# Optimization experiments

Measured on AMD Instinct MI355X. Metric: run time of the kernel, lower is better.

## Reference

```python
import jax, jax.numpy as jnp
import numpy as np

# Static DAG: input -> L hidden layers of K nodes (dense between layers) -> output.
B, WIDTH, K, L = 262144, 64, 4, 4


def _linear_init(key, shape, fan_in):
    # matches nn.Linear default: U(-1/sqrt(fan_in), 1/sqrt(fan_in))
    bound = 1.0 / np.sqrt(fan_in)
    return jax.random.uniform(key, shape, jnp.float32, -bound, bound)


def setup_inputs() -> dict:
    key = jax.random.key(0)
    ks = jax.random.split(key, 9)
    x = jax.random.normal(ks[0], (B, WIDTH), jnp.float32)
    # input node -> first hidden layer (K edges)
    W_in = _linear_init(ks[1], (K, WIDTH, WIDTH), WIDTH)
    b_in = _linear_init(ks[2], (K, WIDTH), WIDTH)
    # between hidden layers: (L-1) transitions, K*K edges each; [pred, node, out, in]
    W_mid = _linear_init(ks[3], (L - 1, K, K, WIDTH, WIDTH), WIDTH)
    b_mid = _linear_init(ks[4], (L - 1, K, K, WIDTH), WIDTH)
    # last hidden layer -> output node (K edges)
    W_out = _linear_init(ks[5], (K, WIDTH, WIDTH), WIDTH)
    b_out = _linear_init(ks[6], (K, WIDTH), WIDTH)
    return {"x": x, "W_in": W_in, "b_in": b_in, "W_mid": W_mid,
            "b_mid": b_mid, "W_out": W_out, "b_out": b_out}


def _l2_normalize(t):
    # torch.linalg.norm(t) with no dim: Frobenius norm over the WHOLE tensor
    return t / jnp.linalg.norm(t)


def reference(x, W_in, b_in, W_mid, b_mid, W_out, b_out):
    # input node -> layer 1: each node k gets a single edge Linear, then normalize
    h = jnp.einsum('bw,kvw->kbv', x, W_in) + b_in[:, None, :]  # [K,B,W]
    h = jax.vmap(_l2_normalize)(h)
    # hidden -> hidden transitions: node v sums over its K predecessor edges
    for l in range(L - 1):  # small fixed structural loop over layers
        pre = jnp.einsum('pbw,pkvw->kbv', h, W_mid[l]) + b_mid[l].sum(axis=0)[:, None, :]
        h = jax.vmap(_l2_normalize)(pre)
    # last layer -> output node: sum K edge outputs, normalize
    out = jnp.einsum('pbw,pvw->bv', h, W_out) + b_out.sum(axis=0)
    return _l2_normalize(out)
```

## Files before the change

kernel.cpp:

```cpp
#include <hip/hip_runtime.h>


#define BF 262144.0f
#define SLOT 4608

#define OFF_G   0
#define OFF_S   4096
#define OFF_P2  8192
#define OFF_C2  73728
#define OFF_P4  74752
#define OFF_C4  91136
#define OFF_MO  91392
#define OFF_CO  95488
#define OFF_X16 98304

typedef __attribute__((ext_vector_type(8))) short bf16x8;
typedef __attribute__((ext_vector_type(4))) float f32x4;
typedef __attribute__((ext_vector_type(4))) unsigned short u16x4;

__device__ __forceinline__ unsigned short f2bf(float f) {
  unsigned u = __builtin_bit_cast(unsigned, f);
  u += 0x7FFF + ((u >> 16) & 1);
  return (unsigned short)(u >> 16);
}
__device__ __forceinline__ float bf2f(unsigned short h) {
  unsigned u = ((unsigned)h) << 16;
  return __builtin_bit_cast(float, u);
}

__device__ __forceinline__ bf16x8 cvt8(f32x4 a, f32x4 b, float s) {
  bf16x8 t;
#pragma unroll
  for (int j = 0; j < 4; j++) {
    t[j]     = (short)f2bf(a[j] * s);
    t[j + 4] = (short)f2bf(b[j] * s);
  }
  return t;
}

__device__ __forceinline__ void split8(f32x4 a, f32x4 b, float sc,
                                       bf16x8& hi, bf16x8& lo) {
#pragma unroll
  for (int j = 0; j < 4; j++) {
    float v = a[j] * sc;
    unsigned short h = f2bf(v);
    hi[j] = (short)h; lo[j] = (short)f2bf(v - bf2f(h));
    v = b[j] * sc;
    h = f2bf(v);
    hi[j + 4] = (short)h; lo[j + 4] = (short)f2bf(v - bf2f(h));
  }
}

__device__ __forceinline__ float qpart(const unsigned short* th,
                                       const unsigned short* tl,
                                       int it, int col, int quad,
                                       const float Greg[4][4]) {
  f32x4 dq[4];
#pragma unroll
  for (int ut = 0; ut < 4; ut++) dq[ut] = (f32x4){0.f, 0.f, 0.f, 0.f};
#pragma unroll
  for (int ks = 0; ks < 2; ks++) {
    const bf16x8 ah = *(const bf16x8*)&th[(it * 16 + col) * 72 + ks * 32 + quad * 8];
    const bf16x8 al = *(const bf16x8*)&tl[(it * 16 + col) * 72 + ks * 32 + quad * 8];
#pragma unroll
    for (int ut = 0; ut < 4; ut++) {
      const bf16x8 bh = *(const bf16x8*)&th[(ut * 16 + col) * 72 + ks * 32 + quad * 8];
      const bf16x8 bl = *(const bf16x8*)&tl[(ut * 16 + col) * 72 + ks * 32 + quad * 8];
      dq[ut] = __builtin_amdgcn_mfma_f32_16x16x32_bf16(ah, bh, dq[ut], 0, 0, 0);
      dq[ut] = __builtin_amdgcn_mfma_f32_16x16x32_bf16(ah, bl, dq[ut], 0, 0, 0);
      dq[ut] = __builtin_amdgcn_mfma_f32_16x16x32_bf16(al, bh, dq[ut], 0, 0, 0);
    }
  }
  float qp = 0.f;
#pragma unroll
  for (int ut = 0; ut < 4; ut++)
#pragma unroll
    for (int r = 0; r < 4; r++) qp += dq[ut][r] * Greg[ut][r];
  return qp;
}

__device__ __forceinline__ void blkred(float qp, float* red4, float* qvv,
                                       int idx, int tid, int lane, int it) {
#pragma unroll
  for (int off = 32; off; off >>= 1) qp += __shfl_down(qp, off, 64);
  if (lane == 0) red4[it] = qp;
  __syncthreads();
  if (tid == 0) qvv[idx] = 1.0f / sqrtf(red4[0] + red4[1] + red4[2] + red4[3]);
  __syncthreads();
}

__global__ __launch_bounds__(256) void kG(const float* __restrict__ x,
                                          float* __restrict__ Gpart,
                                          unsigned short* __restrict__ x16) {
  __shared__ __align__(16) unsigned short xts[4][4][16][8];
  __shared__ float sred[256][4];
  const int tid = threadIdx.x;
  const int lane = tid & 63, mt = tid >> 6;
  const int col = lane & 15, q = lane >> 4;
  const int row0 = tid >> 4;
  const int cf0  = (tid & 15) * 4;

  f32x4 acc[4];
#pragma unroll
  for (int nt = 0; nt < 4; nt++) acc[nt] = (f32x4){0.f, 0.f, 0.f, 0.f};
  float s0 = 0.f, s1 = 0.f, s2 = 0.f, s3 = 0.f;

  const long brow = (long)blockIdx.x * 512;
  const float* bx = x + brow * 64;
  f32x4 r0 = *(const f32x4*)(bx + tid * 4);
  f32x4 r1 = *(const f32x4*)(bx + 1024 + tid * 4);

  for (int c = 0; c < 16; c++) {
    __syncthreads();
    s0 += r0[0] + r1[0]; s1 += r0[1] + r1[1];
    s2 += r0[2] + r1[2]; s3 += r0[3] + r1[3];
    u16x4 h0, h1;
#pragma unroll
    for (int j = 0; j < 4; j++) {
      const int cf = cf0 + j;
      const unsigned short b0 = f2bf(r0[j]);
      const unsigned short b1 = f2bf(r1[j]);
      h0[j] = b0; h1[j] = b1;
      xts[cf >> 4][row0 >> 3][cf & 15][row0 & 7]        = b0;
      xts[cf >> 4][2 + (row0 >> 3)][cf & 15][row0 & 7]  = b1;
    }
    *(u16x4*)(x16 + (brow + c * 32 + row0) * 64 + cf0)      = h0;
    *(u16x4*)(x16 + (brow + c * 32 + 16 + row0) * 64 + cf0) = h1;
    f32x4 r0n = r0, r1n = r1;
    if (c < 15) {
      r0n = *(const f32x4*)(bx + (c + 1) * 2048 + tid * 4);
      r1n = *(const f32x4*)(bx + (c + 1) * 2048 + 1024 + tid * 4);
    }
    __syncthreads();
    const bf16x8 af = *(const bf16x8*)xts[mt][q][col];
#pragma unroll
    for (int nt = 0; nt < 4; nt++) {
      const bf16x8 bfr = *(const bf16x8*)xts[nt][q][col];
      acc[nt] = __builtin_amdgcn_mfma_f32_16x16x32_bf16(af, bfr, acc[nt], 0, 0, 0);
    }
    r0 = r0n; r1 = r1n;
  }

  float* myp = Gpart + (long)blockIdx.x * 4160;
#pragma unroll
  for (int nt = 0; nt < 4; nt++)
#pragma unroll
    for (int r = 0; r < 4; r++)
      myp[(mt * 16 + q * 4 + r) * 64 + nt * 16 + col] = acc[nt][r];

  sred[tid][0] = s0; sred[tid][1] = s1; sred[tid][2] = s2; sred[tid][3] = s3;
  __syncthreads();
  if (tid < 64) {
    float t = 0.f;
#pragma unroll
    for (int k2 = 0; k2 < 16; k2++) t += sred[(tid >> 2) + 16 * k2][tid & 3];
    myp[4096 + tid] = t;
  }
}

__global__ __launch_bounds__(256) void kGred(const float* __restrict__ Gpart,
                                             float* __restrict__ G,
                                             float* __restrict__ s) {
  __shared__ float red[4][64];
  const int tid = threadIdx.x;
  const int e = blockIdx.x * 64 + (tid & 63);
  const int quarter = tid >> 6;
  float acc = 0.f;
#pragma unroll 4
  for (int j = 0; j < 128; j++)
    acc += Gpart[(long)(quarter * 128 + j) * 4160 + e];
  red[quarter][tid & 63] = acc;
  __syncthreads();
  if (tid < 64) {
    const float t = red[0][tid] + red[1][tid] + red[2][tid] + red[3][tid];
    const int ee = blockIdx.x * 64 + tid;
    if (ee < 4096) G[ee] = t;
    else           s[ee - 4096] = t;
  }
}

__global__ __launch_bounds__(256) void kChainA(
    const float* __restrict__ Win, const float* __restrict__ bin,
    const float* __restrict__ Wm0, const float* __restrict__ bm0,
    const float* __restrict__ Wm1, const float* __restrict__ bm1,
    const float* __restrict__ G, const float* __restrict__ s,
    float* __restrict__ Pout, float* __restrict__ cpout) {
  extern __shared__ __align__(16) char smem[];
  unsigned short* Tth = (unsigned short*)smem;
  unsigned short* Ttl = Tth + 4 * SLOT;
  float* cAv  = (float*)(Ttl + 4 * SLOT);
  float* cBv  = cAv + 256;
  float* slv  = cBv + 64;
  float* red4 = slv + 64;
  float* qvv  = red4 + 4;
  float* Tf   = qvv + 8;

  const int tid = threadIdx.x;
  const int p2 = blockIdx.x >> 2, k2 = blockIdx.x & 3;
  const int lane = tid & 63, it = tid >> 6;
  const int col = lane & 15, quad = lane >> 4;

  float Greg[4][4];
#pragma unroll
  for (int ut = 0; ut < 4; ut++)
#pragma unroll
    for (int r = 0; r < 4; r++)
      Greg[ut][r] = G[(it * 16 + quad * 4 + r) * 64 + ut * 16 + col];
  if (tid < 64) slv[tid] = s[tid];
  if (tid < 256) cAv[tid] = bin[tid];

  for (int p = 0; p < 4; p++) {
#pragma unroll
    for (int m = 0; m < 4; m++) {
      const int li = m * 1024 + tid * 4;
      *(f32x4*)&Tf[(li >> 6) * 68 + (li & 63)] = *(const f32x4*)(Win + p * 4096 + li);
    }
    __syncthreads();
    const int tc = tid >> 2, rb = (tid & 3) * 16;
#pragma unroll
    for (int j = 0; j < 16; j++) {
      const float tv = Tf[(rb + j) * 68 + tc];
      const unsigned short h = f2bf(tv);
      Tth[p * SLOT + tc * 72 + rb + j] = h;
      Ttl[p * SLOT + tc * 72 + rb + j] = f2bf(tv - bf2f(h));
    }
    __syncthreads();
  }

#pragma unroll
  for (int p = 0; p < 4; p++) {
    float qp = qpart(Tth + p * SLOT, Ttl + p * SLOT, it, col, quad, Greg);
    if (tid < 64) {
      float sd = 0.f;
      for (int w = 0; w < 64; w++)
        sd += slv[w] * (bf2f(Tth[p * SLOT + w * 72 + tid]) +
                        bf2f(Ttl[p * SLOT + w * 72 + tid]));
      const float c = cAv[p * 64 + tid];
      qp += c * (2.f * sd + BF * c);
    }
    blkred(qp, red4, qvv, p, tid, lane, it);
  }

  f32x4 dc[4];
#pragma unroll
  for (int nt = 0; nt < 4; nt++) dc[nt] = (f32x4){0.f, 0.f, 0.f, 0.f};
  float c2acc = 0.f;

  const int arow = it * 16 + col;
  f32x4 wr[4];
  {
    const float* wbase = Wm0 + (long)((0 * 4 + p2) * 64 + arow) * 64;
    wr[0] = *(const f32x4*)(wbase + quad * 8);
    wr[1] = *(const f32x4*)(wbase + quad * 8 + 4);
    wr[2] = *(const f32x4*)(wbase + 32 + quad * 8);
    wr[3] = *(const f32x4*)(wbase + 36 + quad * 8);
  }
#pragma unroll
  for (int p = 0; p < 4; p++) {
    const float inv = qvv[p];
    bf16x8 awh0, awl0, awh1, awl1;
    split8(wr[0], wr[1], inv, awh0, awl0);
    split8(wr[2], wr[3], inv, awh1, awl1);
    if (p < 3) {
      const float* wbase = Wm0 + (long)(((p + 1) * 4 + p2) * 64 + arow) * 64;
      wr[0] = *(const f32x4*)(wbase + quad * 8);
      wr[1] = *(const f32x4*)(wbase + quad * 8 + 4);
      wr[2] = *(const f32x4*)(wbase + 32 + quad * 8);
      wr[3] = *(const f32x4*)(wbase + 36 + quad * 8);
    }
#pragma unroll
    for (int nt = 0; nt < 4; nt++) {
      const bf16x8 bh0 = *(const bf16x8*)&Tth[p * SLOT + (nt * 16 + col) * 72 + quad * 8];
      const bf16x8 bl0 = *(const bf16x8*)&Ttl[p * SLOT + (nt * 16 + col) * 72 + quad * 8];
      dc[nt] = __builtin_amdgcn_mfma_f32_16x16x32_bf16(awh0, bh0, dc[nt], 0, 0, 0);
      dc[nt] = __builtin_amdgcn_mfma_f32_16x16x32_bf16(awh0, bl0, dc[nt], 0, 0, 0);
      dc[nt] = __builtin_amdgcn_mfma_f32_16x16x32_bf16(awl0, bh0, dc[nt], 0, 0, 0);
      const bf16x8 bh1 = *(const bf16x8*)&Tth[p * SLOT + (nt * 16 + col) * 72 + 32 + quad * 8];
      const bf16x8 bl1 = *(const bf16x8*)&Ttl[p * SLOT + (nt * 16 + col) * 72 + 32 + quad * 8];
      dc[nt] = __builtin_amdgcn_mfma_f32_16x16x32_bf16(awh1, bh1, dc[nt], 0, 0, 0);
      dc[nt] = __builtin_amdgcn_mfma_f32_16x16x32_bf16(awh1, bl1, dc[nt], 0, 0, 0);
      dc[nt] = __builtin_amdgcn_mfma_f32_16x16x32_bf16(awl1, bh1, dc[nt], 0, 0, 0);
    }
    if (tid < 64) {
      const float* wrow = Wm0 + (long)((p * 4 + p2) * 64 + tid) * 64;
      float pc = 0.f;
#pragma unroll
      for (int u4 = 0; u4 < 16; u4++) {
        const f32x4 wv = *(const f32x4*)(wrow + u4 * 4);
        pc += wv[0] * cAv[p * 64 + u4 * 4]     + wv[1] * cAv[p * 64 + u4 * 4 + 1] +
              wv[2] * cAv[p * 64 + u4 * 4 + 2] + wv[3] * cAv[p * 64 + u4 * 4 + 3];
      }
      c2acc += inv * pc + bm0[(p * 4 + p2) * 64 + tid];
    }
  }
  __syncthreads();

#pragma unroll
  for (int nt = 0; nt < 4; nt++)
#pragma unroll
    for (int r = 0; r < 4; r++) {
      const float val = dc[nt][r];
      const unsigned short h = f2bf(val);
      const int w_ = nt * 16 + col, v_ = it * 16 + quad * 4 + r;
      Tth[w_ * 72 + v_] = h;
      Ttl[w_ * 72 + v_] = f2bf(val - bf2f(h));
    }
  if (tid < 64) cBv[tid] = c2acc;
  __syncthreads();

  {
    float qp = qpart(Tth, Ttl, it, col, quad, Greg);
    if (tid < 64) {
      float sd = 0.f;
      for (int w = 0; w < 64; w++)
        sd += slv[w] * (bf2f(Tth[w * 72 + tid]) + bf2f(Ttl[w * 72 + tid]));
      const float c = cBv[tid];
      qp += c * (2.f * sd + BF * c);
    }
    blkred(qp, red4, qvv, 4, tid, lane, it);
  }
  const float inv2 = qvv[4];

  {
    f32x4 dcO[4];
#pragma unroll
    for (int nt = 0; nt < 4; nt++) dcO[nt] = (f32x4){0.f, 0.f, 0.f, 0.f};
    const float* wbase = Wm1 + (long)((p2 * 4 + k2) * 64 + arow) * 64;
    const f32x4 w0 = *(const f32x4*)(wbase + quad * 8);
    const f32x4 w1 = *(const f32x4*)(wbase + quad * 8 + 4);
    const f32x4 w2 = *(const f32x4*)(wbase + 32 + quad * 8);
    const f32x4 w3 = *(const f32x4*)(wbase + 36 + quad * 8);
    bf16x8 awh0, awl0, awh1, awl1;
    split8(w0, w1, inv2, awh0, awl0);
    split8(w2, w3, inv2, awh1, awl1);
#pragma unroll
    for (int nt = 0; nt < 4; nt++) {
      const bf16x8 bh0 = *(const bf16x8*)&Tth[(nt * 16 + col) * 72 + quad * 8];
      const bf16x8 bl0 = *(const bf16x8*)&Ttl[(nt * 16 + col) * 72 + quad * 8];
      dcO[nt] = __builtin_amdgcn_mfma_f32_16x16x32_bf16(awh0, bh0, dcO[nt], 0, 0, 0);
      dcO[nt] = __builtin_amdgcn_mfma_f32_16x16x32_bf16(awh0, bl0, dcO[nt], 0, 0, 0);
      dcO[nt] = __builtin_amdgcn_mfma_f32_16x16x32_bf16(awl0, bh0, dcO[nt], 0, 0, 0);
      const bf16x8 bh1 = *(const bf16x8*)&Tth[(nt * 16 + col) * 72 + 32 + quad * 8];
      const bf16x8 bl1 = *(const bf16x8*)&Ttl[(nt * 16 + col) * 72 + 32 + quad * 8];
      dcO[nt] = __builtin_amdgcn_mfma_f32_16x16x32_bf16(awh1, bh1, dcO[nt], 0, 0, 0);
      dcO[nt] = __builtin_amdgcn_mfma_f32_16x16x32_bf16(awh1, bl1, dcO[nt], 0, 0, 0);
      dcO[nt] = __builtin_amdgcn_mfma_f32_16x16x32_bf16(awl1, bh1, dcO[nt], 0, 0, 0);
    }
    float* po = Pout + (long)(p2 * 4 + k2) * 4096;
#pragma unroll
    for (int nt = 0; nt < 4; nt++)
#pragma unroll
      for (int r = 0; r < 4; r++)
        po[(it * 16 + quad * 4 + r) * 64 + nt * 16 + col] = dcO[nt][r];
    if (tid < 64) {
      const float* wrow = Wm1 + (long)((p2 * 4 + k2) * 64 + tid) * 64;
      float pc = 0.f;
#pragma unroll
      for (int u4 = 0; u4 < 16; u4++) {
        const f32x4 wv = *(const f32x4*)(wrow + u4 * 4);
        pc += wv[0] * cBv[u4 * 4]     + wv[1] * cBv[u4 * 4 + 1] +
              wv[2] * cBv[u4 * 4 + 2] + wv[3] * cBv[u4 * 4 + 3];
      }
      cpout[(p2 * 4 + k2) * 64 + tid] = inv2 * pc + bm1[(p2 * 4 + k2) * 64 + tid];
    }
  }
}

__global__ __launch_bounds__(256) void kChainB(
    const float* __restrict__ Pin, const float* __restrict__ cpin,
    const float* __restrict__ Wm2, const float* __restrict__ bm2,
    const float* __restrict__ Wout, const float* __restrict__ bout,
    const float* __restrict__ G, const float* __restrict__ s,
    float* __restrict__ Pout, float* __restrict__ cpout) {
  extern __shared__ __align__(16) char smem[];
  unsigned short* Tth = (unsigned short*)smem;
  unsigned short* Ttl = Tth + 4 * SLOT;
  float* cAv  = (float*)(Ttl + 4 * SLOT);
  float* cBv  = cAv + 256;
  float* slv  = cBv + 64;
  float* red4 = slv + 64;
  float* qvv  = red4 + 4;
  float* Tf   = qvv + 8;

  const int tid = threadIdx.x;
  const int kp = blockIdx.x;
  const int lane = tid & 63, it = tid >> 6;
  const int col = lane & 15, quad = lane >> 4;

  float Greg[4][4];
#pragma unroll
  for (int ut = 0; ut < 4; ut++)
#pragma unroll
    for (int r = 0; r < 4; r++)
      Greg[ut][r] = G[(it * 16 + quad * 4 + r) * 64 + ut * 16 + col];
  if (tid < 64) slv[tid] = s[tid];
  if (tid < 256) {
    const int k = tid >> 6, v = tid & 63;
    cAv[tid] = cpin[(0 * 4 + k) * 64 + v] + cpin[(1 * 4 + k) * 64 + v] +
               cpin[(2 * 4 + k) * 64 + v] + cpin[(3 * 4 + k) * 64 + v];
  }

  for (int k = 0; k < 4; k++) {
#pragma unroll
    for (int m = 0; m < 4; m++) {
      const int li = m * 1024 + tid * 4;
      const f32x4 a = *(const f32x4*)(Pin + (0 * 4 + k) * 4096 + li);
      const f32x4 b = *(const f32x4*)(Pin + (1 * 4 + k) * 4096 + li);
      const f32x4 c = *(const f32x4*)(Pin + (2 * 4 + k) * 4096 + li);
      const f32x4 d = *(const f32x4*)(Pin + (3 * 4 + k) * 4096 + li);
      *(f32x4*)&Tf[(li >> 6) * 68 + (li & 63)] = a + b + c + d;
    }
    __syncthreads();
    const int tc = tid >> 2, rb = (tid & 3) * 16;
#pragma unroll
    for (int j = 0; j < 16; j++) {
      const float tv = Tf[(rb + j) * 68 + tc];
      const unsigned short h = f2bf(tv);
      Tth[k * SLOT + tc * 72 + rb + j] = h;
      Ttl[k * SLOT + tc * 72 + rb + j] = f2bf(tv - bf2f(h));
    }
    __syncthreads();
  }

#pragma unroll
  for (int k = 0; k < 4; k++) {
    float qp = qpart(Tth + k * SLOT, Ttl + k * SLOT, it, col, quad, Greg);
    if (tid < 64) {
      float sd = 0.f;
      for (int w = 0; w < 64; w++)
        sd += slv[w] * (bf2f(Tth[k * SLOT + w * 72 + tid]) +
                        bf2f(Ttl[k * SLOT + w * 72 + tid]));
      const float c = cAv[k * 64 + tid];
      qp += c * (2.f * sd + BF * c);
    }
    blkred(qp, red4, qvv, k, tid, lane, it);
  }

  f32x4 dc[4];
#pragma unroll
  for (int nt = 0; nt < 4; nt++) dc[nt] = (f32x4){0.f, 0.f, 0.f, 0.f};
  float c4acc = 0.f;

  const int arow = it * 16 + col;
  f32x4 wr[4];
  {
    const float* wbase = Wm2 + (long)((0 * 4 + kp) * 64 + arow) * 64;
    wr[0] = *(const f32x4*)(wbase + quad * 8);
    wr[1] = *(const f32x4*)(wbase + quad * 8 + 4);
    wr[2] = *(const f32x4*)(wbase + 32 + quad * 8);
    wr[3] = *(const f32x4*)(wbase + 36 + quad * 8);
  }
#pragma unroll
  for (int k = 0; k < 4; k++) {
    const float inv = qvv[k];
    bf16x8 awh0, awl0, awh1, awl1;
    split8(wr[0], wr[1], inv, awh0, awl0);
    split8(wr[2], wr[3], inv, awh1, awl1);
    if (k < 3) {
      const float* wbase = Wm2 + (long)(((k + 1) * 4 + kp) * 64 + arow) * 64;
      wr[0] = *(const f32x4*)(wbase + quad * 8);
      wr[1] = *(const f32x4*)(wbase + quad * 8 + 4);
      wr[2] = *(const f32x4*)(wbase + 32 + quad * 8);
      wr[3] = *(const f32x4*)(wbase + 36 + quad * 8);
    }
#pragma unroll
    for (int nt = 0; nt < 4; nt++) {
      const bf16x8 bh0 = *(const bf16x8*)&Tth[k * SLOT + (nt * 16 + col) * 72 + quad * 8];
      const bf16x8 bl0 = *(const bf16x8*)&Ttl[k * SLOT + (nt * 16 + col) * 72 + quad * 8];
      dc[nt] = __builtin_amdgcn_mfma_f32_16x16x32_bf16(awh0, bh0, dc[nt], 0, 0, 0);
      dc[nt] = __builtin_amdgcn_mfma_f32_16x16x32_bf16(awh0, bl0, dc[nt], 0, 0, 0);
      dc[nt] = __builtin_amdgcn_mfma_f32_16x16x32_bf16(awl0, bh0, dc[nt], 0, 0, 0);
      const bf16x8 bh1 = *(const bf16x8*)&Tth[k * SLOT + (nt * 16 + col) * 72 + 32 + quad * 8];
      const bf16x8 bl1 = *(const bf16x8*)&Ttl[k * SLOT + (nt * 16 + col) * 72 + 32 + quad * 8];
      dc[nt] = __builtin_amdgcn_mfma_f32_16x16x32_bf16(awh1, bh1, dc[nt], 0, 0, 0);
      dc[nt] = __builtin_amdgcn_mfma_f32_16x16x32_bf16(awh1, bl1, dc[nt], 0, 0, 0);
      dc[nt] = __builtin_amdgcn_mfma_f32_16x16x32_bf16(awl1, bh1, dc[nt], 0, 0, 0);
    }
    if (tid < 64) {
      const float* wrow = Wm2 + (long)((k * 4 + kp) * 64 + tid) * 64;
      float pc = 0.f;
#pragma unroll
      for (int u4 = 0; u4 < 16; u4++) {
        const f32x4 wv = *(const f32x4*)(wrow + u4 * 4);
        pc += wv[0] * cAv[k * 64 + u4 * 4]     + wv[1] * cAv[k * 64 + u4 * 4 + 1] +
              wv[2] * cAv[k * 64 + u4 * 4 + 2] + wv[3] * cAv[k * 64 + u4 * 4 + 3];
      }
      c4acc += inv * pc + bm2[(k * 4 + kp) * 64 + tid];
    }
  }
  __syncthreads();

#pragma unroll
  for (int nt = 0; nt < 4; nt++)
#pragma unroll
    for (int r = 0; r < 4; r++) {
      const float val = dc[nt][r];
      const unsigned short h = f2bf(val);
      const int w_ = nt * 16 + col, v_ = it * 16 + quad * 4 + r;
      Tth[w_ * 72 + v_] = h;
      Ttl[w_ * 72 + v_] = f2bf(val - bf2f(h));
    }
  if (tid < 64) cBv[tid] = c4acc;
  __syncthreads();

  {
    float qp = qpart(Tth, Ttl, it, col, quad, Greg);
    if (tid < 64) {
      float sd = 0.f;
      for (int w = 0; w < 64; w++)
        sd += slv[w] * (bf2f(Tth[w * 72 + tid]) + bf2f(Ttl[w * 72 + tid]));
      const float c = cBv[tid];
      qp += c * (2.f * sd + BF * c);
    }
    blkred(qp, red4, qvv, 4, tid, lane, it);
  }
  const float inv4 = qvv[4];

  {
    f32x4 dcO[4];
#pragma unroll
    for (int nt = 0; nt < 4; nt++) dcO[nt] = (f32x4){0.f, 0.f, 0.f, 0.f};
    const float* wbase = Wout + (long)(kp * 64 + arow) * 64;
    const f32x4 w0 = *(const f32x4*)(wbase + quad * 8);
    const f32x4 w1 = *(const f32x4*)(wbase + quad * 8 + 4);
    const f32x4 w2 = *(const f32x4*)(wbase + 32 + quad * 8);
    const f32x4 w3 = *(const f32x4*)(wbase + 36 + quad * 8);
    bf16x8 awh0, awl0, awh1, awl1;
    split8(w0, w1, inv4, awh0, awl0);
    split8(w2, w3, inv4, awh1, awl1);
#pragma unroll
    for (int nt = 0; nt < 4; nt++) {
      const bf16x8 bh0 = *(const bf16x8*)&Tth[(nt * 16 + col) * 72 + quad * 8];
      const bf16x8 bl0 = *(const bf16x8*)&Ttl[(nt * 16 + col) * 72 + quad * 8];
      dcO[nt] = __builtin_amdgcn_mfma_f32_16x16x32_bf16(awh0, bh0, dcO[nt], 0, 0, 0);
      dcO[nt] = __builtin_amdgcn_mfma_f32_16x16x32_bf16(awh0, bl0, dcO[nt], 0, 0, 0);
      dcO[nt] = __builtin_amdgcn_mfma_f32_16x16x32_bf16(awl0, bh0, dcO[nt], 0, 0, 0);
      const bf16x8 bh1 = *(const bf16x8*)&Tth[(nt * 16 + col) * 72 + 32 + quad * 8];
      const bf16x8 bl1 = *(const bf16x8*)&Ttl[(nt * 16 + col) * 72 + 32 + quad * 8];
      dcO[nt] = __builtin_amdgcn_mfma_f32_16x16x32_bf16(awh1, bh1, dcO[nt], 0, 0, 0);
      dcO[nt] = __builtin_amdgcn_mfma_f32_16x16x32_bf16(awh1, bl1, dcO[nt], 0, 0, 0);
      dcO[nt] = __builtin_amdgcn_mfma_f32_16x16x32_bf16(awl1, bh1, dcO[nt], 0, 0, 0);
    }
    float* po = Pout + (long)kp * 4096;
#pragma unroll
    for (int nt = 0; nt < 4; nt++)
#pragma unroll
      for (int r = 0; r < 4; r++)
        po[(it * 16 + quad * 4 + r) * 64 + nt * 16 + col] = dcO[nt][r];
    if (tid < 64) {
      const float* wrow = Wout + (long)(kp * 64 + tid) * 64;
      float pc = 0.f;
#pragma unroll
      for (int u4 = 0; u4 < 16; u4++) {
        const f32x4 wv = *(const f32x4*)(wrow + u4 * 4);
        pc += wv[0] * cBv[u4 * 4]     + wv[1] * cBv[u4 * 4 + 1] +
              wv[2] * cBv[u4 * 4 + 2] + wv[3] * cBv[u4 * 4 + 3];
      }
      cpout[kp * 64 + tid] = inv4 * pc + bout[kp * 64 + tid];
    }
  }
}

__global__ __launch_bounds__(256) void kNorm(const float* __restrict__ Psrc,
                                             const float* __restrict__ csrc,
                                             const float* __restrict__ G,
                                             const float* __restrict__ s,
                                             float* __restrict__ MoS,
                                             float* __restrict__ coS) {
  __shared__ float Tf[64][68];
  __shared__ __align__(16) unsigned short Tth[64][68], Ttl[64][68];
  __shared__ float red[256];
  __shared__ __align__(16) float cl[64], sl[64];
  const int tid = threadIdx.x;
  const int lane = tid & 63, it = tid >> 6;
  const int col = lane & 15, quad = lane >> 4;

  float Greg[4][4];
#pragma unroll
  for (int ut = 0; ut < 4; ut++)
#pragma unroll
    for (int r = 0; r < 4; r++)
      Greg[ut][r] = G[(it * 16 + quad * 4 + r) * 64 + ut * 16 + col];

#pragma unroll
  for (int m = 0; m < 16; m++) {
    const int li = m * 256 + tid;
    Tf[li >> 6][li & 63] = Psrc[li] + Psrc[4096 + li] + Psrc[8192 + li] + Psrc[12288 + li];
  }
  if (tid < 64) {
    cl[tid] = csrc[tid] + csrc[64 + tid] + csrc[128 + tid] + csrc[192 + tid];
    sl[tid] = s[tid];
  }
  __syncthreads();

  {
    const int tc = tid >> 2;
    const int rb = (tid & 3) * 16;
#pragma unroll
    for (int j = 0; j < 16; j++) {
      const float tv = Tf[rb + j][tc];
      const unsigned short h = f2bf(tv);
      Tth[tc][rb + j] = h;
      Ttl[tc][rb + j] = f2bf(tv - bf2f(h));
    }
  }
  __syncthreads();

  float qp = 0.f;
  {
    f32x4 dq[4];
#pragma unroll
    for (int ut = 0; ut < 4; ut++) dq[ut] = (f32x4){0.f, 0.f, 0.f, 0.f};
#pragma unroll
    for (int ks = 0; ks < 2; ks++) {
      const bf16x8 ah = *(const bf16x8*)&Tth[it * 16 + col][ks * 32 + quad * 8];
      const bf16x8 al = *(const bf16x8*)&Ttl[it * 16 + col][ks * 32 + quad * 8];
#pragma unroll
      for (int ut = 0; ut < 4; ut++) {
        const bf16x8 bh = *(const bf16x8*)&Tth[ut * 16 + col][ks * 32 + quad * 8];
        const bf16x8 bl = *(const bf16x8*)&Ttl[ut * 16 + col][ks * 32 + quad * 8];
        dq[ut] = __builtin_amdgcn_mfma_f32_16x16x32_bf16(ah, bh, dq[ut], 0, 0, 0);
        dq[ut] = __builtin_amdgcn_mfma_f32_16x16x32_bf16(ah, bl, dq[ut], 0, 0, 0);
        dq[ut] = __builtin_amdgcn_mfma_f32_16x16x32_bf16(al, bh, dq[ut], 0, 0, 0);
      }
    }
#pragma unroll
    for (int ut = 0; ut < 4; ut++)
#pragma unroll
      for (int r = 0; r < 4; r++)
        qp += dq[ut][r] * Greg[ut][r];
  }
  if (tid < 64) {
    float sd = 0.f;
#pragma unroll
    for (int u4 = 0; u4 < 16; u4++) {
      const f32x4 tv = *(const f32x4*)&Tf[tid][u4 * 4];
      const f32x4 sv = *(const f32x4*)&sl[u4 * 4];
      sd += sv[0] * tv[0] + sv[1] * tv[1] + sv[2] * tv[2] + sv[3] * tv[3];
    }
    qp += cl[tid] * (2.f * sd + BF * cl[tid]);
  }
  red[tid] = qp;
  __syncthreads();
  for (int st = 128; st > 0; st >>= 1) {
    if (tid < st) red[tid] += red[tid + st];
    __syncthreads();
  }
  const float inv = 1.0f / sqrtf(red[0]);

#pragma unroll
  for (int m = 0; m < 16; m++) {
    const int li = m * 256 + tid;
    MoS[li] = inv * Tf[li >> 6][li & 63];
  }
  if (tid < 64) coS[tid] = inv * cl[tid];
}

__global__ __launch_bounds__(256) void kApply(const unsigned short* __restrict__ x16,
                                              const float* __restrict__ MoS,
                                              const float* __restrict__ coS,
                                              float* __restrict__ out) {
  const int tid = threadIdx.x, lane = tid & 63, vt = tid >> 6;
  const int col = lane & 15, q = lane >> 4;

  bf16x8 bfr[2];
  const float* mr = MoS + (vt * 16 + col) * 64 + q * 8;
  bfr[0] = cvt8(*(const f32x4*)mr, *(const f32x4*)(mr + 4), 1.f);
  bfr[1] = cvt8(*(const f32x4*)(mr + 32), *(const f32x4*)(mr + 36), 1.f);
  const float cf = coS[vt * 16 + col];

  for (int t = 0; t < 16; t++) {
    const int b0 = (blockIdx.x * 16 + t) * 16;
    const unsigned short* xr = x16 + (long)(b0 + col) * 64 + q * 8;
    const bf16x8 a0 = *(const bf16x8*)xr;
    const bf16x8 a1 = *(const bf16x8*)(xr + 32);
    f32x4 acc = (f32x4){0.f, 0.f, 0.f, 0.f};
    acc = __builtin_amdgcn_mfma_f32_16x16x32_bf16(a0, bfr[0], acc, 0, 0, 0);
    acc = __builtin_amdgcn_mfma_f32_16x16x32_bf16(a1, bfr[1], acc, 0, 0, 0);
#pragma unroll
    for (int r = 0; r < 4; r++)
      out[(long)(b0 + q * 4 + r) * 64 + vt * 16 + col] = acc[r] + cf;
  }
}

extern "C" void kernel_launch(void* const* d_in, const int* in_sizes, int n_in,
                              void* d_out, int out_size, void* d_ws, size_t ws_size,
                              hipStream_t stream) {
  const float* x    = (const float*)d_in[0];
  const float* Win  = (const float*)d_in[1];
  const float* bin  = (const float*)d_in[2];
  const float* Wmid = (const float*)d_in[3];
  const float* bmid = (const float*)d_in[4];
  const float* Wout = (const float*)d_in[5];
  const float* bout = (const float*)d_in[6];
  float* out = (float*)d_out;
  float* ws  = (float*)d_ws;
  float* Gpart = out;
  unsigned short* x16 = (unsigned short*)(ws + OFF_X16);

  const size_t SMEM = (size_t)(8 * SLOT) * 2 + (396 + 8 + 64 * 68) * 4 + 64;
  hipFuncSetAttribute((const void*)kChainA,
                      hipFuncAttributeMaxDynamicSharedMemorySize, (int)SMEM);
  hipFuncSetAttribute((const void*)kChainB,
                      hipFuncAttributeMaxDynamicSharedMemorySize, (int)SMEM);

  kG   <<<512, 256, 0, stream>>>(x, Gpart, x16);
  kGred<<<65, 256, 0, stream>>>(Gpart, ws + OFF_G, ws + OFF_S);
  kChainA<<<16, 256, SMEM, stream>>>(Win, bin, Wmid, bmid, Wmid + 65536, bmid + 1024,
                                     ws + OFF_G, ws + OFF_S, ws + OFF_P2, ws + OFF_C2);
  kChainB<<<4, 256, SMEM, stream>>>(ws + OFF_P2, ws + OFF_C2,
                                    Wmid + 131072, bmid + 2048, Wout, bout,
                                    ws + OFF_G, ws + OFF_S, ws + OFF_P4, ws + OFF_C4);
  kNorm<<<1, 256, 0, stream>>>(ws + OFF_P4, ws + OFF_C4, ws + OFF_G, ws + OFF_S,
                               ws + OFF_MO, ws + OFF_CO);
  kApply<<<1024, 256, 0, stream>>>(x16, ws + OFF_MO, ws + OFF_CO, out);
}
```

Before: 226.8 us.

## Fuse reduction, chain and norm kernels into one cooperative kernel with grid syncs

Replaces the four small serial launches (partial-G reduction, chainA, chainB, norm) with a single cooperative kernel of 65 blocks that separates the stages with grid-wide syncs and thread fences. The goal is to remove the launch gaps between tiny dependent kernels. In exchange, most blocks sit idle in later stages, and every stage now pays for grid barriers and a cooperative launch. The norm stage now uses the shared dynamic smem layout and a qpart helper.

```diff
diff --git a/kernel.cpp b/kernel.cpp
--- a/kernel.cpp
+++ b/kernel.cpp
@@ -1,5 +1,8 @@
 #include <hip/hip_runtime.h>
-
+#include <hip/hip_cooperative_groups.h>
+
+
+namespace cg = cooperative_groups;
 
 #define BF 262144.0f
 #define SLOT 4608
@@ -158,34 +161,12 @@
   }
 }
 
-__global__ __launch_bounds__(256) void kGred(const float* __restrict__ Gpart,
-                                             float* __restrict__ G,
-                                             float* __restrict__ s) {
-  __shared__ float red[4][64];
-  const int tid = threadIdx.x;
-  const int e = blockIdx.x * 64 + (tid & 63);
-  const int quarter = tid >> 6;
-  float acc = 0.f;
-#pragma unroll 4
-  for (int j = 0; j < 128; j++)
-    acc += Gpart[(long)(quarter * 128 + j) * 4160 + e];
-  red[quarter][tid & 63] = acc;
-  __syncthreads();
-  if (tid < 64) {
-    const float t = red[0][tid] + red[1][tid] + red[2][tid] + red[3][tid];
-    const int ee = blockIdx.x * 64 + tid;
-    if (ee < 4096) G[ee] = t;
-    else           s[ee - 4096] = t;
-  }
-}
-
-__global__ __launch_bounds__(256) void kChainA(
+__device__ void chainA_body(char* smem,
     const float* __restrict__ Win, const float* __restrict__ bin,
     const float* __restrict__ Wm0, const float* __restrict__ bm0,
     const float* __restrict__ Wm1, const float* __restrict__ bm1,
     const float* __restrict__ G, const float* __restrict__ s,
-    float* __restrict__ Pout, float* __restrict__ cpout) {
-  extern __shared__ __align__(16) char smem[];
+    float* __restrict__ Pout, float* __restrict__ cpout, int bid) {
   unsigned short* Tth = (unsigned short*)smem;
   unsigned short* Ttl = Tth + 4 * SLOT;
   float* cAv  = (float*)(Ttl + 4 * SLOT);
@@ -196,7 +177,7 @@
   float* Tf   = qvv + 8;
 
   const int tid = threadIdx.x;
-  const int p2 = blockIdx.x >> 2, k2 = blockIdx.x & 3;
+  const int p2 = bid >> 2, k2 = bid & 3;
   const int lane = tid & 63, it = tid >> 6;
   const int col = lane & 15, quad = lane >> 4;
 
@@ -366,13 +347,12 @@
   }
 }
 
-__global__ __launch_bounds__(256) void kChainB(
+__device__ void chainB_body(char* smem,
     const float* __restrict__ Pin, const float* __restrict__ cpin,
     const float* __restrict__ Wm2, const float* __restrict__ bm2,
     const float* __restrict__ Wout, const float* __restrict__ bout,
     const float* __restrict__ G, const float* __restrict__ s,
-    float* __restrict__ Pout, float* __restrict__ cpout) {
-  extern __shared__ __align__(16) char smem[];
+    float* __restrict__ Pout, float* __restrict__ cpout, int bid) {
   unsigned short* Tth = (unsigned short*)smem;
   unsigned short* Ttl = Tth + 4 * SLOT;
   float* cAv  = (float*)(Ttl + 4 * SLOT);
@@ -383,7 +363,7 @@
   float* Tf   = qvv + 8;
 
   const int tid = threadIdx.x;
-  const int kp = blockIdx.x;
+  const int kp = bid;
   const int lane = tid & 63, it = tid >> 6;
   const int col = lane & 15, quad = lane >> 4;
 
@@ -561,16 +541,20 @@
   }
 }
 
-__global__ __launch_bounds__(256) void kNorm(const float* __restrict__ Psrc,
-                                             const float* __restrict__ csrc,
-                                             const float* __restrict__ G,
-                                             const float* __restrict__ s,
-                                             float* __restrict__ MoS,
-                                             float* __restrict__ coS) {
-  __shared__ float Tf[64][68];
-  __shared__ __align__(16) unsigned short Tth[64][68], Ttl[64][68];
-  __shared__ float red[256];
-  __shared__ __align__(16) float cl[64], sl[64];
+__device__ void norm_body(char* smem,
+                          const float* __restrict__ Psrc,
+                          const float* __restrict__ csrc,
+                          const float* __restrict__ G,
+                          const float* __restrict__ s,
+                          float* __restrict__ MoS,
+                          float* __restrict__ coS) {
+  unsigned short* Tth = (unsigned short*)smem;
+  unsigned short* Ttl = Tth + 4 * SLOT;
+  float* red = (float*)(Ttl + 4 * SLOT);
+  float* cl  = red + 256;
+  float* sl  = cl + 64;
+  float* Tf  = sl + 64 + 4 + 8;
+
   const int tid = threadIdx.x;
   const int lane = tid & 63, it = tid >> 6;
   const int col = lane & 15, quad = lane >> 4;
@@ -585,7 +569,8 @@
 #pragma unroll
   for (int m = 0; m < 16; m++) {
     const int li = m * 256 + tid;
-    Tf[li >> 6][li & 63] = Psrc[li] + Psrc[4096 + li] + Psrc[8192 + li] + Psrc[12288 + li];
+    Tf[(li >> 6) * 68 + (li & 63)] =
+        Psrc[li] + Psrc[4096 + li] + Psrc[8192 + li] + Psrc[12288 + li];
   }
   if (tid < 64) {
     cl[tid] = csrc[tid] + csrc[64 + tid] + csrc[128 + tid] + csrc[192 + tid];
@@ -598,43 +583,20 @@
     const int rb = (tid & 3) * 16;
 #pragma unroll
     for (int j = 0; j < 16; j++) {
-      const float tv = Tf[rb + j][tc];
+      const float tv = Tf[(rb + j) * 68 + tc];
       const unsigned short h = f2bf(tv);
-      Tth[tc][rb + j] = h;
-      Ttl[tc][rb + j] = f2bf(tv - bf2f(h));
-    }
-  }
-  __syncthreads();
-
-  float qp = 0.f;
-  {
-    f32x4 dq[4];
-#pragma unroll
-    for (int ut = 0; ut < 4; ut++) dq[ut] = (f32x4){0.f, 0.f, 0.f, 0.f};
-#pragma unroll
-    for (int ks = 0; ks < 2; ks++) {
-      const bf16x8 ah = *(const bf16x8*)&Tth[it * 16 + col][ks * 32 + quad * 8];
-      const bf16x8 al = *(const bf16x8*)&Ttl[it * 16 + col][ks * 32 + quad * 8];
-#pragma unroll
-      for (int ut = 0; ut < 4; ut++) {
-        const bf16x8 bh = *(const bf16x8*)&Tth[ut * 16 + col][ks * 32 + quad * 8];
-        const bf16x8 bl = *(const bf16x8*)&Ttl[ut * 16 + col][ks * 32 + quad * 8];
-        dq[ut] = __builtin_amdgcn_mfma_f32_16x16x32_bf16(ah, bh, dq[ut], 0, 0, 0);
-        dq[ut] = __builtin_amdgcn_mfma_f32_16x16x32_bf16(ah, bl, dq[ut], 0, 0, 0);
-        dq[ut] = __builtin_amdgcn_mfma_f32_16x16x32_bf16(al, bh, dq[ut], 0, 0, 0);
-      }
-    }
-#pragma unroll
-    for (int ut = 0; ut < 4; ut++)
-#pragma unroll
-      for (int r = 0; r < 4; r++)
-        qp += dq[ut][r] * Greg[ut][r];
-  }
+      Tth[tc * 72 + rb + j] = h;
+      Ttl[tc * 72 + rb + j] = f2bf(tv - bf2f(h));
+    }
+  }
+  __syncthreads();
+
+  float qp = qpart(Tth, Ttl, it, col, quad, Greg);
   if (tid < 64) {
     float sd = 0.f;
 #pragma unroll
     for (int u4 = 0; u4 < 16; u4++) {
-      const f32x4 tv = *(const f32x4*)&Tf[tid][u4 * 4];
+      const f32x4 tv = *(const f32x4*)&Tf[tid * 68 + u4 * 4];
       const f32x4 sv = *(const f32x4*)&sl[u4 * 4];
       sd += sv[0] * tv[0] + sv[1] * tv[1] + sv[2] * tv[2] + sv[3] * tv[3];
     }
@@ -651,9 +613,59 @@
 #pragma unroll
   for (int m = 0; m < 16; m++) {
     const int li = m * 256 + tid;
-    MoS[li] = inv * Tf[li >> 6][li & 63];
+    MoS[li] = inv * Tf[(li >> 6) * 68 + (li & 63)];
   }
   if (tid < 64) coS[tid] = inv * cl[tid];
+}
+
+__global__ __launch_bounds__(256) void kFused(
+    const float* __restrict__ Gpart,
+    const float* __restrict__ Win, const float* __restrict__ bin,
+    const float* __restrict__ Wmid, const float* __restrict__ bmid,
+    const float* __restrict__ Wout, const float* __restrict__ bout,
+    float* __restrict__ ws) {
+  extern __shared__ __align__(16) char smem[];
+  float* G  = ws + OFF_G;  float* s  = ws + OFF_S;
+  float* P2 = ws + OFF_P2; float* C2 = ws + OFF_C2;
+  float* P4 = ws + OFF_P4; float* C4 = ws + OFF_C4;
+  float* MO = ws + OFF_MO; float* CO = ws + OFF_CO;
+  const int tid = threadIdx.x;
+
+  {
+    float (*redm)[64] = (float(*)[64])smem;
+    const int vb = blockIdx.x;
+    const int e = vb * 64 + (tid & 63);
+    const int quarter = tid >> 6;
+    float acc = 0.f;
+#pragma unroll 4
+    for (int j = 0; j < 128; j++)
+      acc += Gpart[(long)(quarter * 128 + j) * 4160 + e];
+    redm[quarter][tid & 63] = acc;
+    __syncthreads();
+    if (tid < 64) {
+      const float t = redm[0][tid] + redm[1][tid] + redm[2][tid] + redm[3][tid];
+      const int ee = vb * 64 + tid;
+      if (ee < 4096) G[ee] = t;
+      else           s[ee - 4096] = t;
+    }
+  }
+  __threadfence();
+  cg::this_grid().sync();
+
+  if (blockIdx.x < 16)
+    chainA_body(smem, Win, bin, Wmid, bmid, Wmid + 65536, bmid + 1024,
+                G, s, P2, C2, blockIdx.x);
+  __threadfence();
+  cg::this_grid().sync();
+
+  if (blockIdx.x < 4)
+    chainB_body(smem, P2, C2, Wmid + 131072, bmid + 2048, Wout, bout,
+                G, s, P4, C4, blockIdx.x);
+  __threadfence();
+  cg::this_grid().sync();
+
+  if (blockIdx.x == 0)
+    norm_body(smem, P4, C4, G, s, MO, CO);
 }
 
 __global__ __launch_bounds__(256) void kApply(const unsigned short* __restrict__ x16,
@@ -699,19 +711,18 @@
   unsigned short* x16 = (unsigned short*)(ws + OFF_X16);
 
   const size_t SMEM = (size_t)(8 * SLOT) * 2 + (396 + 8 + 64 * 68) * 4 + 64;
-  hipFuncSetAttribute((const void*)kChainA,
+  hipFuncSetAttribute((const void*)kFused,
                       hipFuncAttributeMaxDynamicSharedMemorySize, (int)SMEM);
-  hipFuncSetAttribute((const void*)kChainB,
-                      hipFuncAttributeMaxDynamicSharedMemorySize, (int)SMEM);
-
-  kG   <<<512, 256, 0, stream>>>(x, Gpart, x16);
-  kGred<<<65, 256, 0, stream>>>(Gpart, ws + OFF_G, ws + OFF_S);
-  kChainA<<<16, 256, SMEM, stream>>>(Win, bin, Wmid, bmid, Wmid + 65536, bmid + 1024,
-                                     ws + OFF_G, ws + OFF_S, ws + OFF_P2, ws + OFF_C2);
-  kChainB<<<4, 256, SMEM, stream>>>(ws + OFF_P2, ws + OFF_C2,
-                                    Wmid + 131072, bmid + 2048, Wout, bout,
-                                    ws + OFF_G, ws + OFF_S, ws + OFF_P4, ws + OFF_C4);
-  kNorm<<<1, 256, 0, stream>>>(ws + OFF_P4, ws + OFF_C4, ws + OFF_G, ws + OFF_S,
-                               ws + OFF_MO, ws + OFF_CO);
+
+  kG<<<512, 256, 0, stream>>>(x, Gpart, x16);
+
+  {
+    const float* gpart_c = (const float*)Gpart;
+    void* args[] = {(void*)&gpart_c, (void*)&Win, (void*)&bin, (void*)&Wmid,
+                    (void*)&bmid, (void*)&Wout, (void*)&bout, (void*)&ws};
+    hipLaunchCooperativeKernel((const void*)kFused, dim3(65), dim3(256),
+                               args, (unsigned)SMEM, stream);
+  }
+
   kApply<<<1024, 256, 0, stream>>>(x16, ws + OFF_MO, ws + OFF_CO, out);
 }
```

After: 284.3 us. 1.25x slower.
